# Kernel tuning notes

Hardware: AMD Instinct MI355X
Metric: run time of the kernel (lower is better)

The kernel has to match this reference:

```python
import jax, jax.numpy as jnp
import numpy as np

T, B, S, A, D = 512, 256, 256, 8, 64
EPS = 1e-6
LOG2PI = float(np.log(2.0 * np.pi))


def setup_inputs() -> dict:
    key = jax.random.key(0)
    ks = jax.random.split(key, 6)
    return {
        "x": jax.random.normal(ks[0], (T, B, D), dtype=jnp.float32),
        "a": jax.random.uniform(ks[1], (T, B, A), dtype=jnp.float32),
        "mask": jnp.ones((T, B), dtype=jnp.float32),
        "mu": jax.random.normal(ks[2], (S, D), dtype=jnp.float32),
        "lv": jax.random.normal(ks[3], (S, D), dtype=jnp.float32) * 0.1,
        "w_logits": jax.random.normal(ks[4], (A, S, S), dtype=jnp.float32),
        "s0_logits": jax.random.normal(ks[5], (S,), dtype=jnp.float32),
    }


def _gauss_log_prob(x, mu, lv):
    # x: [T,B,D], mu/lv: [S,D] -> [T,B,S]; diagonal Gaussian via matmul expansion
    inv_var = jnp.exp(-lv)                                  # [S,D]
    quad = (jnp.einsum('tbd,sd->tbs', x * x, inv_var)
            - 2.0 * jnp.einsum('tbd,sd->tbs', x, mu * inv_var)
            + jnp.sum(mu * mu * inv_var, axis=-1))          # [T,B,S]
    return -0.5 * (quad + jnp.sum(lv, axis=-1) + D * LOG2PI)


def reference(x, a, mask, mu, lv, w_logits, s0_logits):
    trans_all = jax.nn.softmax(w_logits, axis=-1)           # [A,S,S] row-stochastic
    log_pi0 = jax.nn.log_softmax(s0_logits)                 # [S]
    logp_x = _gauss_log_prob(x, mu, lv)                     # [T,B,S]

    # ---- forward (alpha) ----
    b1 = jax.nn.softmax(logp_x[0] + log_pi0[None, :], axis=-1)  # [B,S]

    def fstep(b, inp):
        lx, a_prev = inp
        trans = jnp.einsum('ba,aij->bij', a_prev, trans_all)      # [B,S,S]
        logp_z = jnp.log(jnp.sum(trans * b[:, :, None] + EPS, axis=1))
        b_t = jax.nn.softmax(lx + logp_z, axis=-1)
        return b_t, b_t

    _, alpha_rest = jax.lax.scan(fstep, b1, (logp_x[1:], a[:-1]))
    alpha = jnp.concatenate([b1[None], alpha_rest], axis=0)       # [T,B,S]

    # ---- backward (log beta) ----
    logb_T = jnp.zeros((B, S), dtype=x.dtype)

    def bstep(logb, inp):
        lx, a_prev, m_t = inp
        trans = jnp.einsum('ba,aij->bij', a_prev, trans_all)      # [B,S,S]
        logb_prev = jax.nn.logsumexp(lx[:, None, :] + jnp.log(trans + EPS)
                                     + logb[:, None, :], axis=-1)
        logb_prev = logb_prev * (m_t[:, None] == 1.0)
        return logb_prev, logb_prev

    _, beta_rest = jax.lax.scan(bstep, logb_T, (logp_x[1:], a[:-1], mask[1:]),
                                reverse=True)
    log_beta = jnp.concatenate([beta_rest, logb_T[None]], axis=0)  # [T,B,S]

    # ---- posterior state marginals ----
    q_z = jax.nn.softmax(jnp.log(alpha + EPS) + log_beta, axis=-1)
    return q_z
```

## Files before the change

kernel.cpp:

```cpp
#include <hip/hip_runtime.h>
#include <hip/hip_bf16.h>

#define TT 512
#define BB 256
#define SS 256
#define AA 8
#define DD 64

typedef unsigned short ushort_t;
typedef unsigned long long u64_t;
typedef __bf16 bf16x8 __attribute__((ext_vector_type(8)));
typedef float  f32x4  __attribute__((ext_vector_type(4)));

__device__ __forceinline__ ushort_t f2bf(float x) {
  union { float f; unsigned u; } v; v.f = x;
  unsigned r = (v.u + 0x7FFFu + ((v.u >> 16) & 1u)) >> 16;
  return (ushort_t)r;
}
__device__ __forceinline__ float bf2f(unsigned h) {
  return __uint_as_float((h & 0xFFFFu) << 16);
}
__device__ __forceinline__ u64_t ld_u64(const u64_t* p) {
  return __hip_atomic_load(p, __ATOMIC_RELAXED, __HIP_MEMORY_SCOPE_AGENT);
}
__device__ __forceinline__ unsigned ld_u32(const unsigned* p) {
  return __hip_atomic_load(p, __ATOMIC_RELAXED, __HIP_MEMORY_SCOPE_AGENT);
}
__device__ __forceinline__ void st_u32(unsigned* p, unsigned v) {
  __hip_atomic_store(p, v, __ATOMIC_RELAXED, __HIP_MEMORY_SCOPE_AGENT);
}

__global__ __launch_bounds__(64) void k_params(const float* __restrict__ mu,
                                               const float* __restrict__ lv,
                                               float* __restrict__ A1, float* __restrict__ A2,
                                               float* __restrict__ Cs) {
  const float LOG2PI = 1.8378770664093453f;
  int s = blockIdx.x, d = threadIdx.x;
  float l = lv[s * DD + d], m_ = mu[s * DD + d];
  float inv = __expf(-l);
  A1[s * DD + d] = inv;
  A2[s * DD + d] = m_ * inv;
  float part = m_ * m_ * inv + l;
  #pragma unroll
  for (int o = 32; o >= 1; o >>= 1) part += __shfl_down(part, o);
  if (d == 0) Cs[s] = part + (float)DD * LOG2PI;
}

__global__ __launch_bounds__(256) void k_pi0(const float* __restrict__ s0, float* __restrict__ lp0) {
  __shared__ float red[4];
  int tid = threadIdx.x, ln = tid & 63, wv = tid >> 6;
  float v = s0[tid];
  float m = v;
  #pragma unroll
  for (int o = 32; o >= 1; o >>= 1) m = fmaxf(m, __shfl_xor(m, o));
  if (ln == 0) red[wv] = m;
  __syncthreads();
  m = fmaxf(fmaxf(red[0], red[1]), fmaxf(red[2], red[3]));
  __syncthreads();
  float e = __expf(v - m);
  float s = e;
  #pragma unroll
  for (int o = 32; o >= 1; o >>= 1) s += __shfl_xor(s, o);
  if (ln == 0) red[wv] = s;
  __syncthreads();
  s = red[0] + red[1] + red[2] + red[3];
  lp0[tid] = v - m - __logf(s);
}

__global__ __launch_bounds__(256) void k_trans(const float* __restrict__ wl,
                                               ushort_t* __restrict__ Wf, ushort_t* __restrict__ Wb) {
  int tid = threadIdx.x;
  int rl = tid >> 5, l = tid & 31;
  int row = blockIdx.x * 8 + rl;
  int a = row >> 8, i = row & 255;
  const float* src = wl + (size_t)row * 256 + l * 8;
  float v[8];
  *reinterpret_cast<float4*>(&v[0]) = *reinterpret_cast<const float4*>(src);
  *reinterpret_cast<float4*>(&v[4]) = *reinterpret_cast<const float4*>(src + 4);
  float m = v[0];
  #pragma unroll
  for (int k = 1; k < 8; ++k) m = fmaxf(m, v[k]);
  #pragma unroll
  for (int o = 16; o >= 1; o >>= 1) m = fmaxf(m, __shfl_xor(m, o, 32));
  float s = 0.f;
  #pragma unroll
  for (int k = 0; k < 8; ++k) { v[k] = __expf(v[k] - m); s += v[k]; }
  #pragma unroll
  for (int o = 16; o >= 1; o >>= 1) s += __shfl_xor(s, o, 32);
  float inv = 1.0f / s;
  #pragma unroll
  for (int k = 0; k < 8; ++k) {
    int j = l * 8 + k;
    ushort_t h = f2bf(v[k] * inv);
    size_t fi = (size_t)((a * 8 + (i >> 5)) * 16 + (j >> 4));
    Wf[fi * 512 + (((i >> 3) & 3) * 16 + (j & 15)) * 8 + (i & 7)] = h;
    size_t bi = (size_t)((a * 8 + (j >> 5)) * 16 + (i >> 4));
    Wb[bi * 512 + (((j >> 3) & 3) * 16 + (i & 15)) * 8 + (j & 7)] = h;
  }
}

__global__ __launch_bounds__(256) void k_logp(const float* __restrict__ x,
    const float* __restrict__ A1, const float* __restrict__ A2,
    const float* __restrict__ Cs, float* __restrict__ logp, float* __restrict__ Mmax) {
  __shared__ float sA1[64][64];
  __shared__ float sA2[64][64];
  int tid = threadIdx.x;
  int row = tid >> 3, dg = tid & 7;
  size_t row0 = (size_t)blockIdx.x * 32;
  const float* xp = x + (row0 + row) * DD + dg * 8;
  float xv[8];
  *reinterpret_cast<float4*>(&xv[0]) = *reinterpret_cast<const float4*>(xp);
  *reinterpret_cast<float4*>(&xv[4]) = *reinterpret_cast<const float4*>(xp + 4);
  float m = -3.0e38f;
  float* orow = logp + (row0 + row) * SS;
  for (int st = 0; st < 4; ++st) {
    __syncthreads();
    #pragma unroll
    for (int k = 0; k < 4; ++k) {
      int flat = k * 1024 + tid * 4;
      int sr = flat >> 6, sc = flat & 63;
      *reinterpret_cast<float4*>(&sA1[sr][sc]) = *reinterpret_cast<const float4*>(&A1[(size_t)(st * 64 + sr) * 64 + sc]);
      *reinterpret_cast<float4*>(&sA2[sr][sc]) = *reinterpret_cast<const float4*>(&A2[(size_t)(st * 64 + sr) * 64 + sc]);
    }
    __syncthreads();
    for (int s = 0; s < 64; ++s) {
      float acc = 0.f;
      #pragma unroll
      for (int j = 0; j < 8; ++j) {
        float t1 = __builtin_fmaf(sA1[s][dg * 8 + j], xv[j], -2.0f * sA2[s][dg * 8 + j]);
        acc = __builtin_fmaf(t1, xv[j], acc);
      }
      acc += __shfl_xor(acc, 1, 8);
      acc += __shfl_xor(acc, 2, 8);
      acc += __shfl_xor(acc, 4, 8);
      float lp = -0.5f * (acc + Cs[st * 64 + s]);
      m = fmaxf(m, lp);
      if (((s ^ dg) & 7) == 0) orow[st * 64 + s] = lp;
    }
  }
  if (dg == 0) Mmax[row0 + row] = m;
}

__global__ __launch_bounds__(256, 1) void k_recur(
    const float* __restrict__ a_in, const float* __restrict__ mask,
    float* __restrict__ out, float* __restrict__ beta,
    const float* __restrict__ logp, const float* __restrict__ Mmax,
    float* __restrict__ cpart,
    const ushort_t* __restrict__ Wf, const ushort_t* __restrict__ Wb,
    const float* __restrict__ lp0,
    unsigned* __restrict__ amb, unsigned* __restrict__ bmb,
    unsigned* __restrict__ cmb, unsigned* __restrict__ rmb) {
  const float EPSF  = 1e-6f;
  const float EPS_S = 256.0f * 1e-6f;
  const int tid  = threadIdx.x;
  const int lane = tid & 63;
  const int wave = tid >> 6;
  const int xcd  = blockIdx.x & 7;
  const int slot = blockIdx.x >> 3;
  const int wg   = slot & 7;
  const int grpg = (slot >> 3) * 8 + xcd;
  const bool isF = (grpg < 16);
  const int grp  = grpg & 15;
  const int b0   = grp * 16;
  const int jc0  = wg * 32;

  __shared__ float yred[2][4][2][64][4];
  __shared__ float rowUp[2][4][16];

  bf16x8 bfrag[8][2][2];
  {
    const ushort_t* Ws = isF ? Wf : Wb;
    #pragma unroll
    for (int a = 0; a < 8; ++a)
      #pragma unroll
      for (int kk = 0; kk < 2; ++kk)
        #pragma unroll
        for (int nt = 0; nt < 2; ++nt) {
          const int kc = wave * 2 + kk;
          const int fragid = (a * 8 + kc) * 16 + wg * 2 + nt;
          bfrag[a][kk][nt] = *reinterpret_cast<const bf16x8*>(Ws + (size_t)fragid * 512 + lane * 8);
        }
  }

  const int m_ = lane & 15;
  const int q_ = lane >> 4;
  const int frow = tid >> 4;
  const int fcol = tid & 15;
  const int lsrc = (frow >> 2) * 16 + fcol;
  const int rg_  = frow & 3;
  const u64_t TAGMASK = 0xFFFF0000FFFF0000ULL;

  if (isF) {
    {
      float mm = Mmax[b0 + frow];
      float csum = 0.f;
      #pragma unroll
      for (int nt = 0; nt < 2; ++nt) {
        int j = jc0 + nt * 16 + fcol;
        float lx = logp[(size_t)(b0 + frow) * SS + j];
        float v = __expf(lx - mm + lp0[j]);
        out[(size_t)(b0 + frow) * SS + j] = v;
        st_u32(&amb[((size_t)(0 * 16 + grp) * 16 + frow) * 256 + j], (unsigned)f2bf(v));
        csum += v;
      }
      #pragma unroll
      for (int o = 8; o >= 1; o >>= 1) csum += __shfl_down(csum, o, 16);
      if (fcol == 0) {
        cpart[((size_t)grp * 16 + frow) * 8 + wg] = csum;
        st_u32(&cmb[((size_t)(0 * 16 + grp) * 16 + frow) * 8 + wg], (unsigned)f2bf(csum));
      }
    }

    for (int t = 1; t < TT; ++t) {
      const int par_r = (t - 1) & 1, par_w = t & 1;
      float wcur[4][8];
      {
        const float* ab = a_in + ((size_t)(t - 1) * BB + b0 + q_ * 4) * AA;
        #pragma unroll
        for (int r = 0; r < 4; ++r) {
          *reinterpret_cast<float4*>(&wcur[r][0]) = *reinterpret_cast<const float4*>(ab + r * AA);
          *reinterpret_cast<float4*>(&wcur[r][4]) = *reinterpret_cast<const float4*>(ab + r * AA + 4);
        }
      }
      float mmn = Mmax[(size_t)t * BB + b0 + frow];
      const float* lsp = logp + ((size_t)t * BB + b0 + frow) * SS + jc0;
      float ex0 = __expf(lsp[fcol] - mmn);
      float ex1 = __expf(lsp[16 + fcol] - mmn);

      const u64_t* pr = (const u64_t*)(amb + (((size_t)par_r * 16 + grp) * 16 + m_) * 256);
      const u64_t* p0 = pr + wave * 32 + q_ * 4;
      const u64_t* p1 = p0 + 16;
      const unsigned* pc  = cmb + (((size_t)par_r * 16 + grp) * 16 + (lane >> 3)) * 8 + (lane & 7);
      const unsigned* pc2 = pc + 64;
      const unsigned tg = (unsigned)(t - 1);
      const u64_t pat = ((u64_t)tg << 48) | ((u64_t)tg << 16);
      u64_t d[8]; unsigned clo, chi;
      while (true) {
        #pragma unroll
        for (int k = 0; k < 4; ++k) { d[k] = ld_u64(p0 + k); d[4 + k] = ld_u64(p1 + k); }
        clo = ld_u32(pc); chi = ld_u32(pc2);
        bool ok = ((clo >> 16) == tg) & ((chi >> 16) == tg);
        #pragma unroll
        for (int k = 0; k < 8; ++k) ok &= ((d[k] & TAGMASK) == pat);
        if (__all(ok)) break;
      }
      float slo = bf2f(clo), shi = bf2f(chi);
      slo += __shfl_xor(slo, 4, 8); slo += __shfl_xor(slo, 2, 8); slo += __shfl_xor(slo, 1, 8);
      shi += __shfl_xor(shi, 4, 8); shi += __shfl_xor(shi, 2, 8); shi += __shfl_xor(shi, 1, 8);
      float vlo = __shfl(slo, (m_ & 7) * 8);
      float vhi = __shfl(shi, (m_ & 7) * 8);
      float ra = 1.0f / ((m_ < 8) ? vlo : vhi);

      float ys[2][4] = {{0.f,0.f,0.f,0.f},{0.f,0.f,0.f,0.f}};
      {
        bf16x8 af0, af1;
        #pragma unroll
        for (int e = 0; e < 8; ++e) {
          unsigned h0 = (e & 1) ? (unsigned)(d[e >> 1] >> 32) : (unsigned)d[e >> 1];
          unsigned h1 = (e & 1) ? (unsigned)(d[4 + (e >> 1)] >> 32) : (unsigned)d[4 + (e >> 1)];
          af0[e] = (__bf16)(bf2f(h0) * ra);
          af1[e] = (__bf16)(bf2f(h1) * ra);
        }
        #pragma unroll
        for (int a = 0; a < 8; ++a) {
          #pragma unroll
          for (int nt = 0; nt < 2; ++nt) {
            f32x4 c = {0.f, 0.f, 0.f, 0.f};
            c = __builtin_amdgcn_mfma_f32_16x16x32_bf16(af0, bfrag[a][0][nt], c, 0, 0, 0);
            c = __builtin_amdgcn_mfma_f32_16x16x32_bf16(af1, bfrag[a][1][nt], c, 0, 0, 0);
            #pragma unroll
            for (int r = 0; r < 4; ++r) ys[nt][r] += wcur[r][a] * c[r];
          }
        }
      }
      #pragma unroll
      for (int nt = 0; nt < 2; ++nt)
        *reinterpret_cast<float4*>(&yred[par_w][wave][nt][lane][0]) =
            make_float4(ys[nt][0], ys[nt][1], ys[nt][2], ys[nt][3]);
      __syncthreads();
      {
        float csum = 0.f;
        float* orow = out + ((size_t)t * BB + b0 + frow) * SS + jc0;
        unsigned* mrow = amb + (((size_t)par_w * 16 + grp) * 16 + frow) * 256 + jc0;
        float y0 = yred[par_w][0][0][lsrc][rg_] + yred[par_w][1][0][lsrc][rg_] +
                   yred[par_w][2][0][lsrc][rg_] + yred[par_w][3][0][lsrc][rg_];
        float bh0 = ex0 * (y0 + EPS_S);
        orow[fcol] = bh0;
        st_u32(mrow + fcol, ((unsigned)t << 16) | f2bf(bh0));
        csum += bh0;
        float y1 = yred[par_w][0][1][lsrc][rg_] + yred[par_w][1][1][lsrc][rg_] +
                   yred[par_w][2][1][lsrc][rg_] + yred[par_w][3][1][lsrc][rg_];
        float bh1 = ex1 * (y1 + EPS_S);
        orow[16 + fcol] = bh1;
        st_u32(mrow + 16 + fcol, ((unsigned)t << 16) | f2bf(bh1));
        csum += bh1;
        #pragma unroll
        for (int o = 8; o >= 1; o >>= 1) csum += __shfl_down(csum, o, 16);
        if (fcol == 0) {
          cpart[(((size_t)t * 16 + grp) * 16 + frow) * 8 + wg] = csum;
          st_u32(&cmb[(((size_t)par_w * 16 + grp) * 16 + frow) * 8 + wg],
                 ((unsigned)t << 16) | f2bf(csum));
        }
      }
    }
  } else {
    {
      const unsigned tg0 = (unsigned)(TT - 1);
      float* brow = beta + ((size_t)(TT - 1) * BB + b0 + frow) * SS + jc0;
      unsigned* mrow = bmb + (((size_t)((TT - 1) & 1) * 16 + grp) * 16 + frow) * 256 + jc0;
      brow[fcol] = 1.0f; brow[16 + fcol] = 1.0f;
      st_u32(mrow + fcol, (tg0 << 16) | 0x3F80u);
      st_u32(mrow + 16 + fcol, (tg0 << 16) | 0x3F80u);
      if (fcol == 0)
        st_u32(&rmb[(((size_t)((TT - 1) & 1) * 16 + grp) * 16 + frow) * 8 + wg],
               (tg0 << 16) | f2bf(32.0f));
    }

    for (int t = TT - 2; t >= 0; --t) {
      const int tr = t + 1;
      const int par_r = tr & 1, par_w = t & 1;
      float wcur[4][8];
      {
        const float* ab = a_in + ((size_t)t * BB + b0 + q_ * 4) * AA;
        #pragma unroll
        for (int r = 0; r < 4; ++r) {
          *reinterpret_cast<float4*>(&wcur[r][0]) = *reinterpret_cast<const float4*>(ab + r * AA);
          *reinterpret_cast<float4*>(&wcur[r][4]) = *reinterpret_cast<const float4*>(ab + r * AA + 4);
        }
      }
      float lp0v[8], lp1v[8];
      {
        const float* lrow = logp + ((size_t)tr * BB + b0 + m_) * SS + wave * 64 + q_ * 8;
        *reinterpret_cast<float4*>(&lp0v[0]) = *reinterpret_cast<const float4*>(lrow);
        *reinterpret_cast<float4*>(&lp0v[4]) = *reinterpret_cast<const float4*>(lrow + 4);
        *reinterpret_cast<float4*>(&lp1v[0]) = *reinterpret_cast<const float4*>(lrow + 32);
        *reinterpret_cast<float4*>(&lp1v[4]) = *reinterpret_cast<const float4*>(lrow + 36);
      }
      float mm_ = Mmax[(size_t)tr * BB + b0 + m_];
      float mk  = mask[(size_t)tr * BB + b0 + frow];

      const u64_t* pr = (const u64_t*)(bmb + (((size_t)par_r * 16 + grp) * 16 + m_) * 256);
      const u64_t* p0 = pr + wave * 32 + q_ * 4;
      const u64_t* p1 = p0 + 16;
      const unsigned* pc  = rmb + (((size_t)par_r * 16 + grp) * 16 + (lane >> 3)) * 8 + (lane & 7);
      const unsigned* pc2 = pc + 64;
      const unsigned tg = (unsigned)tr;
      const u64_t pat = ((u64_t)tg << 48) | ((u64_t)tg << 16);
      u64_t d[8]; unsigned clo, chi;
      while (true) {
        #pragma unroll
        for (int k = 0; k < 4; ++k) { d[k] = ld_u64(p0 + k); d[4 + k] = ld_u64(p1 + k); }
        clo = ld_u32(pc); chi = ld_u32(pc2);
        bool ok = ((clo >> 16) == tg) & ((chi >> 16) == tg);
        #pragma unroll
        for (int k = 0; k < 8; ++k) ok &= ((d[k] & TAGMASK) == pat);
        if (__all(ok)) break;
      }
      float slo = bf2f(clo), shi = bf2f(chi);
      slo += __shfl_xor(slo, 4, 8); slo += __shfl_xor(slo, 2, 8); slo += __shfl_xor(slo, 1, 8);
      shi += __shfl_xor(shi, 4, 8); shi += __shfl_xor(shi, 2, 8); shi += __shfl_xor(shi, 1, 8);
      float vlo = __shfl(slo, (m_ & 7) * 8);
      float vhi = __shfl(shi, (m_ & 7) * 8);
      float ri = 1.0f / ((m_ < 8) ? vlo : vhi);
      float vloF = __shfl(slo, (frow & 7) * 8);
      float vhiF = __shfl(shi, (frow & 7) * 8);
      float riF = 1.0f / ((frow < 8) ? vloF : vhiF);

      float partial = 0.f;
      float ys[2][4] = {{0.f,0.f,0.f,0.f},{0.f,0.f,0.f,0.f}};
      {
        bf16x8 af0, af1;
        #pragma unroll
        for (int e = 0; e < 8; ++e) {
          unsigned h0 = (e & 1) ? (unsigned)(d[e >> 1] >> 32) : (unsigned)d[e >> 1];
          unsigned h1 = (e & 1) ? (unsigned)(d[4 + (e >> 1)] >> 32) : (unsigned)d[4 + (e >> 1)];
          float g0 = __expf(lp0v[e] - mm_) * bf2f(h0);
          float g1 = __expf(lp1v[e] - mm_) * bf2f(h1);
          partial += g0 + g1;
          af0[e] = (__bf16)(g0 * ri);
          af1[e] = (__bf16)(g1 * ri);
        }
        #pragma unroll
        for (int a = 0; a < 8; ++a) {
          #pragma unroll
          for (int nt = 0; nt < 2; ++nt) {
            f32x4 c = {0.f, 0.f, 0.f, 0.f};
            c = __builtin_amdgcn_mfma_f32_16x16x32_bf16(af0, bfrag[a][0][nt], c, 0, 0, 0);
            c = __builtin_amdgcn_mfma_f32_16x16x32_bf16(af1, bfrag[a][1][nt], c, 0, 0, 0);
            #pragma unroll
            for (int r = 0; r < 4; ++r) ys[nt][r] += wcur[r][a] * c[r];
          }
        }
      }
      partial += __shfl_xor(partial, 16);
      partial += __shfl_xor(partial, 32);
      if (q_ == 0) rowUp[par_w][wave][m_] = partial;
      #pragma unroll
      for (int nt = 0; nt < 2; ++nt)
        *reinterpret_cast<float4*>(&yred[par_w][wave][nt][lane][0]) =
            make_float4(ys[nt][0], ys[nt][1], ys[nt][2], ys[nt][3]);
      __syncthreads();
      {
        float rowU = rowUp[par_w][0][frow] + rowUp[par_w][1][frow] +
                     rowUp[par_w][2][frow] + rowUp[par_w][3][frow];
        float eg = EPSF * riF * rowU;
        bool mk1 = (mk == 1.0f);
        float rsum = 0.f;
        float* brow = beta + ((size_t)t * BB + b0 + frow) * SS + jc0;
        unsigned* mrow = bmb + (((size_t)par_w * 16 + grp) * 16 + frow) * 256 + jc0;
        #pragma unroll
        for (int nt = 0; nt < 2; ++nt) {
          float y = yred[par_w][0][nt][lsrc][rg_] + yred[par_w][1][nt][lsrc][rg_] +
                    yred[par_w][2][nt][lsrc][rg_] + yred[par_w][3][nt][lsrc][rg_];
          float val = mk1 ? (y + eg) : 1.0f;
          brow[nt * 16 + fcol] = val;
          st_u32(mrow + nt * 16 + fcol, ((unsigned)t << 16) | f2bf(val));
          rsum += val;
        }
        #pragma unroll
        for (int o = 8; o >= 1; o >>= 1) rsum += __shfl_down(rsum, o, 16);
        if (fcol == 0)
          st_u32(&rmb[(((size_t)par_w * 16 + grp) * 16 + frow) * 8 + wg],
                 ((unsigned)t << 16) | f2bf(rsum));
      }
    }
  }
}

__global__ __launch_bounds__(256) void k_qz(float* __restrict__ out,
    const float* __restrict__ beta, const float* __restrict__ cpart) {
  const float EPSF = 1e-6f;
  int tid = threadIdx.x;
  size_t row = (size_t)blockIdx.x * 8 + (tid >> 5);
  int l = tid & 31;
  int tt = (int)(row >> 8);
  int b  = (int)(row & 255);
  int grp = b >> 4, r = b & 15;
  float pv = 0.f;
  if (l < 8) pv = cpart[(((size_t)tt * 16 + grp) * 16 + r) * 8 + l];
  pv += __shfl_down(pv, 4, 8); pv += __shfl_down(pv, 2, 8); pv += __shfl_down(pv, 1, 8);
  float ce = __shfl(pv, 0, 32) * EPSF;
  float* po = out + row * SS + l * 8;
  const float* pb = beta + row * SS + l * 8;
  float4 v0 = *reinterpret_cast<const float4*>(po);
  float4 v1 = *reinterpret_cast<const float4*>(po + 4);
  float4 b0 = *reinterpret_cast<const float4*>(pb);
  float4 b1 = *reinterpret_cast<const float4*>(pb + 4);
  float z[8];
  z[0] = __logf(v0.x + ce) + __logf(b0.x);
  z[1] = __logf(v0.y + ce) + __logf(b0.y);
  z[2] = __logf(v0.z + ce) + __logf(b0.z);
  z[3] = __logf(v0.w + ce) + __logf(b0.w);
  z[4] = __logf(v1.x + ce) + __logf(b1.x);
  z[5] = __logf(v1.y + ce) + __logf(b1.y);
  z[6] = __logf(v1.z + ce) + __logf(b1.z);
  z[7] = __logf(v1.w + ce) + __logf(b1.w);
  float m = z[0];
  #pragma unroll
  for (int k = 1; k < 8; ++k) m = fmaxf(m, z[k]);
  #pragma unroll
  for (int o = 16; o >= 1; o >>= 1) m = fmaxf(m, __shfl_xor(m, o, 32));
  float e[8]; float s = 0.f;
  #pragma unroll
  for (int k = 0; k < 8; ++k) { e[k] = __expf(z[k] - m); s += e[k]; }
  #pragma unroll
  for (int o = 16; o >= 1; o >>= 1) s += __shfl_xor(s, o, 32);
  float inv = 1.0f / s;
  *reinterpret_cast<float4*>(po)     = make_float4(e[0]*inv, e[1]*inv, e[2]*inv, e[3]*inv);
  *reinterpret_cast<float4*>(po + 4) = make_float4(e[4]*inv, e[5]*inv, e[6]*inv, e[7]*inv);
}

extern "C" void kernel_launch(void* const* d_in, const int* in_sizes, int n_in,
                              void* d_out, int out_size, void* d_ws, size_t ws_size,
                              hipStream_t stream) {
  (void)in_sizes; (void)n_in; (void)out_size;
  const float* x   = (const float*)d_in[0];
  const float* a   = (const float*)d_in[1];
  const float* msk = (const float*)d_in[2];
  const float* mu  = (const float*)d_in[3];
  const float* lv  = (const float*)d_in[4];
  const float* wl  = (const float*)d_in[5];
  const float* s0  = (const float*)d_in[6];
  float* out = (float*)d_out;

  char* ws = (char*)d_ws;
  float* logp  = (float*)ws;  ws += (size_t)TT * BB * SS * 4;
  float* beta  = (float*)ws;  ws += (size_t)TT * BB * SS * 4;
  float* Mmax  = (float*)ws;  ws += (size_t)TT * BB * 4;
  float* cpart = (float*)ws;  ws += (size_t)TT * BB * 8 * 4;
  ushort_t* Wf = (ushort_t*)ws; ws += (size_t)AA * SS * SS * 2;
  ushort_t* Wb = (ushort_t*)ws; ws += (size_t)AA * SS * SS * 2;
  float* A1 = (float*)ws;    ws += (size_t)SS * DD * 4;
  float* A2 = (float*)ws;    ws += (size_t)SS * DD * 4;
  float* Cs = (float*)ws;    ws += 1024;
  float* lp0 = (float*)ws;   ws += 1024;
  unsigned* amb = (unsigned*)ws; ws += (size_t)2 * 16 * 16 * 256 * 4;
  unsigned* bmb = (unsigned*)ws; ws += (size_t)2 * 16 * 16 * 256 * 4;
  unsigned* cmb = (unsigned*)ws; ws += (size_t)2 * 16 * 16 * 8 * 4;
  unsigned* rmb = (unsigned*)ws; ws += (size_t)2 * 16 * 16 * 8 * 4;
  if (ws_size < (size_t)(ws - (char*)d_ws)) return;

  hipMemsetAsync(amb, 0xFF, (size_t)(2 * 16 * 16 * 256 * 4) * 2 + (size_t)(2 * 16 * 16 * 8 * 4) * 2, stream);

  k_params<<<SS, DD, 0, stream>>>(mu, lv, A1, A2, Cs);
  k_pi0<<<1, SS, 0, stream>>>(s0, lp0);
  k_trans<<<256, 256, 0, stream>>>(wl, Wf, Wb);
  k_logp<<<TT * BB / 32, 256, 0, stream>>>(x, A1, A2, Cs, logp, Mmax);
  k_recur<<<256, 256, 0, stream>>>(a, msk, out, beta, logp, Mmax, cpart, Wf, Wb, lp0,
                                   amb, bmb, cmb, rmb);
  k_qz<<<TT * BB / 8, 256, 0, stream>>>(out, beta, cpart);
}
```

Before: 2.274 ms.

## Poll only row-sum mailbox flags, then load tagged data after release fence

The spin-wait in the recurrence now polls only the small per-row sum mailbox. It loads the 256-wide tagged bf16 data only after that flag is observed, and a vmcnt wait before each flag store orders the data stores ahead of it. Bulk traffic on logp, the output, beta and cpart switches to nontemporal loads and stores to reduce cache pollution, and the memset covers only the flag mailboxes. This cuts per-iteration polling traffic on the serial critical path. The risk is ordering: a relaxed atomic store after s_waitcnt may not guarantee the data is visible to other CUs at agent scope without cache writeback semantics.

```diff
diff --git a/kernel.cpp b/kernel.cpp
--- a/kernel.cpp
+++ b/kernel.cpp
@@ -28,6 +28,9 @@
 }
 __device__ __forceinline__ void st_u32(unsigned* p, unsigned v) {
   __hip_atomic_store(p, v, __ATOMIC_RELAXED, __HIP_MEMORY_SCOPE_AGENT);
+}
+__device__ __forceinline__ void release_fence() {
+  asm volatile("s_waitcnt vmcnt(0)" ::: "memory");
 }
 
 __global__ __launch_bounds__(64) void k_params(const float* __restrict__ mu,
@@ -135,7 +138,7 @@
       acc += __shfl_xor(acc, 4, 8);
       float lp = -0.5f * (acc + Cs[st * 64 + s]);
       m = fmaxf(m, lp);
-      if (((s ^ dg) & 7) == 0) orow[st * 64 + s] = lp;
+      if (((s ^ dg) & 7) == 0) __builtin_nontemporal_store(lp, orow + st * 64 + s);
     }
   }
   if (dg == 0) Mmax[row0 + row] = m;
@@ -188,7 +191,6 @@
   const int fcol = tid & 15;
   const int lsrc = (frow >> 2) * 16 + fcol;
   const int rg_  = frow & 3;
-  const u64_t TAGMASK = 0xFFFF0000FFFF0000ULL;
 
   if (isF) {
     {
@@ -197,16 +199,17 @@
       #pragma unroll
       for (int nt = 0; nt < 2; ++nt) {
         int j = jc0 + nt * 16 + fcol;
-        float lx = logp[(size_t)(b0 + frow) * SS + j];
+        float lx = __builtin_nontemporal_load(logp + (size_t)(b0 + frow) * SS + j);
         float v = __expf(lx - mm + lp0[j]);
-        out[(size_t)(b0 + frow) * SS + j] = v;
+        __builtin_nontemporal_store(v, out + (size_t)(b0 + frow) * SS + j);
         st_u32(&amb[((size_t)(0 * 16 + grp) * 16 + frow) * 256 + j], (unsigned)f2bf(v));
         csum += v;
       }
       #pragma unroll
       for (int o = 8; o >= 1; o >>= 1) csum += __shfl_down(csum, o, 16);
       if (fcol == 0) {
-        cpart[((size_t)grp * 16 + frow) * 8 + wg] = csum;
+        __builtin_nontemporal_store(csum, &cpart[((size_t)grp * 16 + frow) * 8 + wg]);
+        release_fence();
         st_u32(&cmb[((size_t)(0 * 16 + grp) * 16 + frow) * 8 + wg], (unsigned)f2bf(csum));
       }
     }
@@ -224,8 +227,10 @@
       }
       float mmn = Mmax[(size_t)t * BB + b0 + frow];
       const float* lsp = logp + ((size_t)t * BB + b0 + frow) * SS + jc0;
-      float ex0 = __expf(lsp[fcol] - mmn);
-      float ex1 = __expf(lsp[16 + fcol] - mmn);
+      float lx0 = __builtin_nontemporal_load(lsp + fcol);
+      float lx1 = __builtin_nontemporal_load(lsp + 16 + fcol);
+      float ex0 = __expf(lx0 - mmn);
+      float ex1 = __expf(lx1 - mmn);
 
       const u64_t* pr = (const u64_t*)(amb + (((size_t)par_r * 16 + grp) * 16 + m_) * 256);
       const u64_t* p0 = pr + wave * 32 + q_ * 4;
@@ -233,17 +238,16 @@
       const unsigned* pc  = cmb + (((size_t)par_r * 16 + grp) * 16 + (lane >> 3)) * 8 + (lane & 7);
       const unsigned* pc2 = pc + 64;
       const unsigned tg = (unsigned)(t - 1);
-      const u64_t pat = ((u64_t)tg << 48) | ((u64_t)tg << 16);
-      u64_t d[8]; unsigned clo, chi;
+      unsigned clo, chi;
       while (true) {
-        #pragma unroll
-        for (int k = 0; k < 4; ++k) { d[k] = ld_u64(p0 + k); d[4 + k] = ld_u64(p1 + k); }
         clo = ld_u32(pc); chi = ld_u32(pc2);
         bool ok = ((clo >> 16) == tg) & ((chi >> 16) == tg);
-        #pragma unroll
-        for (int k = 0; k < 8; ++k) ok &= ((d[k] & TAGMASK) == pat);
         if (__all(ok)) break;
       }
+      __builtin_amdgcn_sched_barrier(0);
+      u64_t d[8];
+      #pragma unroll
+      for (int k = 0; k < 4; ++k) { d[k] = ld_u64(p0 + k); d[4 + k] = ld_u64(p1 + k); }
       float slo = bf2f(clo), shi = bf2f(chi);
       slo += __shfl_xor(slo, 4, 8); slo += __shfl_xor(slo, 2, 8); slo += __shfl_xor(slo, 1, 8);
       shi += __shfl_xor(shi, 4, 8); shi += __shfl_xor(shi, 2, 8); shi += __shfl_xor(shi, 1, 8);
@@ -285,19 +289,20 @@
         float y0 = yred[par_w][0][0][lsrc][rg_] + yred[par_w][1][0][lsrc][rg_] +
                    yred[par_w][2][0][lsrc][rg_] + yred[par_w][3][0][lsrc][rg_];
         float bh0 = ex0 * (y0 + EPS_S);
-        orow[fcol] = bh0;
+        __builtin_nontemporal_store(bh0, orow + fcol);
         st_u32(mrow + fcol, ((unsigned)t << 16) | f2bf(bh0));
         csum += bh0;
         float y1 = yred[par_w][0][1][lsrc][rg_] + yred[par_w][1][1][lsrc][rg_] +
                    yred[par_w][2][1][lsrc][rg_] + yred[par_w][3][1][lsrc][rg_];
         float bh1 = ex1 * (y1 + EPS_S);
-        orow[16 + fcol] = bh1;
+        __builtin_nontemporal_store(bh1, orow + 16 + fcol);
         st_u32(mrow + 16 + fcol, ((unsigned)t << 16) | f2bf(bh1));
         csum += bh1;
         #pragma unroll
         for (int o = 8; o >= 1; o >>= 1) csum += __shfl_down(csum, o, 16);
         if (fcol == 0) {
-          cpart[(((size_t)t * 16 + grp) * 16 + frow) * 8 + wg] = csum;
+          __builtin_nontemporal_store(csum, &cpart[(((size_t)t * 16 + grp) * 16 + frow) * 8 + wg]);
+          release_fence();
           st_u32(&cmb[(((size_t)par_w * 16 + grp) * 16 + frow) * 8 + wg],
                  ((unsigned)t << 16) | f2bf(csum));
         }
@@ -308,12 +313,15 @@
       const unsigned tg0 = (unsigned)(TT - 1);
       float* brow = beta + ((size_t)(TT - 1) * BB + b0 + frow) * SS + jc0;
       unsigned* mrow = bmb + (((size_t)((TT - 1) & 1) * 16 + grp) * 16 + frow) * 256 + jc0;
-      brow[fcol] = 1.0f; brow[16 + fcol] = 1.0f;
+      __builtin_nontemporal_store(1.0f, brow + fcol);
+      __builtin_nontemporal_store(1.0f, brow + 16 + fcol);
       st_u32(mrow + fcol, (tg0 << 16) | 0x3F80u);
       st_u32(mrow + 16 + fcol, (tg0 << 16) | 0x3F80u);
-      if (fcol == 0)
+      if (fcol == 0) {
+        release_fence();
         st_u32(&rmb[(((size_t)((TT - 1) & 1) * 16 + grp) * 16 + frow) * 8 + wg],
                (tg0 << 16) | f2bf(32.0f));
+      }
     }
 
     for (int t = TT - 2; t >= 0; --t) {
@@ -345,17 +353,16 @@
       const unsigned* pc  = rmb + (((size_t)par_r * 16 + grp) * 16 + (lane >> 3)) * 8 + (lane & 7);
       const unsigned* pc2 = pc + 64;
       const unsigned tg = (unsigned)tr;
-      const u64_t pat = ((u64_t)tg << 48) | ((u64_t)tg << 16);
-      u64_t d[8]; unsigned clo, chi;
+      unsigned clo, chi;
       while (true) {
-        #pragma unroll
-        for (int k = 0; k < 4; ++k) { d[k] = ld_u64(p0 + k); d[4 + k] = ld_u64(p1 + k); }
         clo = ld_u32(pc); chi = ld_u32(pc2);
         bool ok = ((clo >> 16) == tg) & ((chi >> 16) == tg);
-        #pragma unroll
-        for (int k = 0; k < 8; ++k) ok &= ((d[k] & TAGMASK) == pat);
         if (__all(ok)) break;
       }
+      __builtin_amdgcn_sched_barrier(0);
+      u64_t d[8];
+      #pragma unroll
+      for (int k = 0; k < 4; ++k) { d[k] = ld_u64(p0 + k); d[4 + k] = ld_u64(p1 + k); }
       float slo = bf2f(clo), shi = bf2f(chi);
       slo += __shfl_xor(slo, 4, 8); slo += __shfl_xor(slo, 2, 8); slo += __shfl_xor(slo, 1, 8);
       shi += __shfl_xor(shi, 4, 8); shi += __shfl_xor(shi, 2, 8); shi += __shfl_xor(shi, 1, 8);
@@ -413,15 +420,17 @@
           float y = yred[par_w][0][nt][lsrc][rg_] + yred[par_w][1][nt][lsrc][rg_] +
                     yred[par_w][2][nt][lsrc][rg_] + yred[par_w][3][nt][lsrc][rg_];
           float val = mk1 ? (y + eg) : 1.0f;
-          brow[nt * 16 + fcol] = val;
+          __builtin_nontemporal_store(val, brow + nt * 16 + fcol);
           st_u32(mrow + nt * 16 + fcol, ((unsigned)t << 16) | f2bf(val));
           rsum += val;
         }
         #pragma unroll
         for (int o = 8; o >= 1; o >>= 1) rsum += __shfl_down(rsum, o, 16);
-        if (fcol == 0)
+        if (fcol == 0) {
+          release_fence();
           st_u32(&rmb[(((size_t)par_w * 16 + grp) * 16 + frow) * 8 + wg],
                  ((unsigned)t << 16) | f2bf(rsum));
+        }
       }
     }
   }
@@ -442,19 +451,19 @@
   float ce = __shfl(pv, 0, 32) * EPSF;
   float* po = out + row * SS + l * 8;
   const float* pb = beta + row * SS + l * 8;
-  float4 v0 = *reinterpret_cast<const float4*>(po);
-  float4 v1 = *reinterpret_cast<const float4*>(po + 4);
-  float4 b0 = *reinterpret_cast<const float4*>(pb);
-  float4 b1 = *reinterpret_cast<const float4*>(pb + 4);
+  f32x4 v0 = __builtin_nontemporal_load(reinterpret_cast<const f32x4*>(po));
+  f32x4 v1 = __builtin_nontemporal_load(reinterpret_cast<const f32x4*>(po + 4));
+  f32x4 b0 = __builtin_nontemporal_load(reinterpret_cast<const f32x4*>(pb));
+  f32x4 b1 = __builtin_nontemporal_load(reinterpret_cast<const f32x4*>(pb + 4));
   float z[8];
-  z[0] = __logf(v0.x + ce) + __logf(b0.x);
-  z[1] = __logf(v0.y + ce) + __logf(b0.y);
-  z[2] = __logf(v0.z + ce) + __logf(b0.z);
-  z[3] = __logf(v0.w + ce) + __logf(b0.w);
-  z[4] = __logf(v1.x + ce) + __logf(b1.x);
-  z[5] = __logf(v1.y + ce) + __logf(b1.y);
-  z[6] = __logf(v1.z + ce) + __logf(b1.z);
-  z[7] = __logf(v1.w + ce) + __logf(b1.w);
+  z[0] = __logf(v0[0] + ce) + __logf(b0[0]);
+  z[1] = __logf(v0[1] + ce) + __logf(b0[1]);
+  z[2] = __logf(v0[2] + ce) + __logf(b0[2]);
+  z[3] = __logf(v0[3] + ce) + __logf(b0[3]);
+  z[4] = __logf(v1[0] + ce) + __logf(b1[0]);
+  z[5] = __logf(v1[1] + ce) + __logf(b1[1]);
+  z[6] = __logf(v1[2] + ce) + __logf(b1[2]);
+  z[7] = __logf(v1[3] + ce) + __logf(b1[3]);
   float m = z[0];
   #pragma unroll
   for (int k = 1; k < 8; ++k) m = fmaxf(m, z[k]);
@@ -466,8 +475,10 @@
   #pragma unroll
   for (int o = 16; o >= 1; o >>= 1) s += __shfl_xor(s, o, 32);
   float inv = 1.0f / s;
-  *reinterpret_cast<float4*>(po)     = make_float4(e[0]*inv, e[1]*inv, e[2]*inv, e[3]*inv);
-  *reinterpret_cast<float4*>(po + 4) = make_float4(e[4]*inv, e[5]*inv, e[6]*inv, e[7]*inv);
+  f32x4 r0 = { e[0]*inv, e[1]*inv, e[2]*inv, e[3]*inv };
+  f32x4 r1 = { e[4]*inv, e[5]*inv, e[6]*inv, e[7]*inv };
+  __builtin_nontemporal_store(r0, reinterpret_cast<f32x4*>(po));
+  __builtin_nontemporal_store(r1, reinterpret_cast<f32x4*>(po + 4));
 }
 
 extern "C" void kernel_launch(void* const* d_in, const int* in_sizes, int n_in,
@@ -500,7 +511,7 @@
   unsigned* rmb = (unsigned*)ws; ws += (size_t)2 * 16 * 16 * 8 * 4;
   if (ws_size < (size_t)(ws - (char*)d_ws)) return;
 
-  hipMemsetAsync(amb, 0xFF, (size_t)(2 * 16 * 16 * 256 * 4) * 2 + (size_t)(2 * 16 * 16 * 8 * 4) * 2, stream);
+  hipMemsetAsync(cmb, 0xFF, (size_t)(2 * 16 * 16 * 8 * 4) * 2, stream);
 
   k_params<<<SS, DD, 0, stream>>>(mu, lv, A1, A2, Cs);
   k_pi0<<<1, SS, 0, stream>>>(s0, lp0);
```

Measured after the change: 3.430 ms. 1.51x slower.
